# Optimization experiments

Hardware: AMD Instinct MI355X
Metric: run time of the kernel (lower is better)

## Reference

```python
import jax, jax.numpy as jnp
import numpy as np

N = 100000   # nodes
E = 640000   # directed edges
D = 128      # feature dim
C = 2        # classes


def setup_inputs() -> dict:
    key = jax.random.key(0)
    ks = jax.random.split(key, 7)
    s = 1.0 / np.sqrt(D)
    return {
        "x": jax.random.normal(ks[0], (N, D), jnp.float32),
        "edge_index": jax.random.randint(ks[1], (2, E), 0, N, jnp.int32),
        "W1": jax.random.normal(ks[2], (D, D), jnp.float32) * s,
        "b1": jnp.zeros((D,), jnp.float32),
        "W2": jax.random.normal(ks[3], (D, D), jnp.float32) * s,
        "b2": jnp.zeros((D,), jnp.float32),
        "Wfc": jax.random.normal(ks[4], (D, C), jnp.float32) * s,
        "bfc": jnp.zeros((C,), jnp.float32),
    }


def _gcn_conv(h, src, dst, W, b, n):
    """PyG GCNConv: y = D^{-1/2}(A+I)D^{-1/2} (h @ W) + b."""
    h = h @ W  # [N, D_out]
    loop = jnp.arange(n, dtype=src.dtype)
    s = jnp.concatenate([src, loop])
    d = jnp.concatenate([dst, loop])
    # degree of (A + I) counted at destination
    deg = jax.ops.segment_sum(jnp.ones_like(d, jnp.float32), d, num_segments=n)
    dinv = jax.lax.rsqrt(jnp.maximum(deg, 1.0))  # deg >= 1 via self loops
    norm = dinv[s] * dinv[d]                      # [E+N]
    msg = h[s] * norm[:, None]                    # gather + scale
    out = jax.ops.segment_sum(msg, d, num_segments=n)  # scatter-add
    return out + b


def reference(x, edge_index, W1, b1, W2, b2, Wfc, bfc):
    src, dst = edge_index[0], edge_index[1]
    n = x.shape[0]
    h = jax.nn.relu(_gcn_conv(x, src, dst, W1, b1, n))  # dropout = identity (eval)
    h = jax.nn.relu(_gcn_conv(h, src, dst, W2, b2, n))
    return h @ Wfc + bfc  # [N, 2] logits
```

## Files before the change

### kernel.cpp

```cpp
#include <hip/hip_runtime.h>
#include <hip/hip_bf16.h>

#define D 128
#define NBUCKET 64
#define BCAP 16384

typedef __bf16 bf16x8 __attribute__((ext_vector_type(8)));
typedef float f32x4 __attribute__((ext_vector_type(4)));


__global__ void prep_kernel(const float* __restrict__ W1, const float* __restrict__ W2,
                            __bf16* __restrict__ pw, int* __restrict__ bucket_cursor,
                            int* __restrict__ deghist, int* __restrict__ degcur) {
    int b = blockIdx.x;
    if (b < 128) {
        int t = b * 256 + threadIdx.x;
        int which = t >> 14, idx = t & 16383;
        const float* W = which ? W2 : W1;
        float w = W[idx];
        int k = idx >> 7, nn = idx & 127;
        int ks = which ? (((k & 15) << 3) | (k >> 4)) : k;
        int ntile = nn >> 4, nl = nn & 15;
        int kchunk = ks >> 5, quad = (ks >> 3) & 3, j = ks & 7;
        int o = (((ntile * 4 + kchunk) * 64 + quad * 16 + nl) << 3) + j;
        pw[(size_t)which * 16384 + o] = (__bf16)w;
    } else {
        int t = threadIdx.x;
        if (t < NBUCKET) bucket_cursor[t] = 0;
        else if (t < 128) deghist[t - 64] = 0;
        else if (t < 192) degcur[t - 128] = 0;
    }
}

__global__ void mega1_kernel(const float* __restrict__ X, const __bf16* __restrict__ PW,
                             __bf16* __restrict__ Zs, int nrows, int gb,
                             const int* __restrict__ src, const int* __restrict__ dst,
                             int* __restrict__ bucket_cursor, int2* __restrict__ bucket_edges,
                             int e, int bucketW) {
    __shared__ __align__(16) char smem[32768];
    int t = threadIdx.x;
    int b = blockIdx.x;
    if (b >= gb) {
        int* hist = (int*)smem;
        int* gbase = hist + 64;
        if (t < NBUCKET) hist[t] = 0;
        __syncthreads();
        int i0 = ((b - gb) * 256 + t) * 4;
        int sv[4], dv[4], bk[4], ls[4];
        int nv = 0;
        if (i0 + 4 <= e) {
            int4 s4 = *(const int4*)(src + i0);
            int4 d4 = *(const int4*)(dst + i0);
            sv[0] = s4.x; sv[1] = s4.y; sv[2] = s4.z; sv[3] = s4.w;
            dv[0] = d4.x; dv[1] = d4.y; dv[2] = d4.z; dv[3] = d4.w;
            nv = 4;
        } else {
            for (int i = i0; i < e; i++) { sv[nv] = src[i]; dv[nv] = dst[i]; nv++; }
        }
        for (int u = 0; u < nv; u++) {
            bk[u] = dv[u] / bucketW;
            ls[u] = atomicAdd(&hist[bk[u]], 1);
        }
        __syncthreads();
        if (t < NBUCKET) gbase[t] = atomicAdd(&bucket_cursor[t], hist[t]);
        __syncthreads();
        for (int u = 0; u < nv; u++) {
            int pos = bk[u] * BCAP + gbase[bk[u]] + ls[u];
            bucket_edges[pos] = make_int2(sv[u], dv[u]);
        }
        return;
    }
    bf16x8* sB = (bf16x8*)smem;
    const bf16x8* PW8 = (const bf16x8*)PW;
#pragma unroll
    for (int i = 0; i < 8; i++) sB[t + 256 * i] = PW8[t + 256 * i];

    int wave = t >> 6, lane = t & 63;
    int qm = lane & 15, quad = lane >> 4;
    int r0 = b * 64 + wave * 16;
    int row = r0 + qm;
    bool valid = row < nrows;
    const float* xr = X + (size_t)row * D + quad * 8;

    bf16x8 ahi[4], alo[4];
#pragma unroll
    for (int c = 0; c < 4; c++) {
        float4 zf = {0.f, 0.f, 0.f, 0.f};
        float4 xa = valid ? ((const float4*)(xr + c * 32))[0] : zf;
        float4 xb = valid ? ((const float4*)(xr + c * 32))[1] : zf;
        float xs[8] = {xa.x, xa.y, xa.z, xa.w, xb.x, xb.y, xb.z, xb.w};
        bf16x8 h, l;
#pragma unroll
        for (int j = 0; j < 8; j++) {
            float v = xs[j];
            __bf16 hh = (__bf16)v;
            h[j] = hh;
            l[j] = (__bf16)(v - (float)hh);
        }
        ahi[c] = h; alo[c] = l;
    }

    f32x4 acc[8];
#pragma unroll
    for (int nt = 0; nt < 8; nt++) acc[nt] = (f32x4){0.f, 0.f, 0.f, 0.f};

    __syncthreads();

#pragma unroll
    for (int c = 0; c < 4; c++) {
#pragma unroll
        for (int nt = 0; nt < 8; nt++) {
            bf16x8 bb = sB[(nt * 4 + c) * 64 + lane];
            acc[nt] = __builtin_amdgcn_mfma_f32_16x16x32_bf16(ahi[c], bb, acc[nt], 0, 0, 0);
            acc[nt] = __builtin_amdgcn_mfma_f32_16x16x32_bf16(alo[c], bb, acc[nt], 0, 0, 0);
        }
    }

#pragma unroll
    for (int reg = 0; reg < 4; reg++) {
        int orow = r0 + quad * 4 + reg;
        if (orow < nrows) {
            bf16x8 o;
#pragma unroll
            for (int nt = 0; nt < 8; nt++) o[nt] = (__bf16)acc[nt][reg];
            *(bf16x8*)(Zs + (size_t)orow * D + qm * 8) = o;
        }
    }
}

__global__ void count2_kernel(const int2* __restrict__ bucket_edges,
                              const int* __restrict__ bucket_cursor,
                              int* __restrict__ counts, float* __restrict__ dinv,
                              int* __restrict__ partial, int* __restrict__ deghist,
                              int n, int bucketW, int subW) {
    __shared__ int bins[400];
    __shared__ int sm[256];
    __shared__ int hb[64];
    int b = blockIdx.x, t = threadIdx.x;
    int bk = b >> 2, j = b & 3;
    int ns = bk * bucketW + j * subW;
    int be = min((bk + 1) * bucketW, n);
    int ne = min(ns + subW, be);
    int w = ne - ns;
    if (w <= 0) { if (t == 0) partial[b] = 0; return; }
    for (int i = t; i < w; i += 256) bins[i] = 0;
    if (t < 64) hb[t] = 0;
    __syncthreads();
    int m = bucket_cursor[bk];
    const int2* eb = bucket_edges + (size_t)bk * BCAP;
    for (int i = t; i < m; i += 256) {
        int d = eb[i].y;
        if (d >= ns && d < ne) atomicAdd(&bins[d - ns], 1);
    }
    __syncthreads();
    int s = 0;
    for (int i = t; i < w; i += 256) {
        int c = bins[i];
        counts[ns + i] = c;
        dinv[ns + i] = rsqrtf((float)(c + 1));
        atomicAdd(&hb[min(c, 63)], 1);
        s += c;
    }
    sm[t] = s; __syncthreads();
    for (int off = 128; off > 0; off >>= 1) { if (t < off) sm[t] += sm[t + off]; __syncthreads(); }
    if (t == 0) partial[b] = sm[0];
    if (t < 64 && hb[t]) atomicAdd(&deghist[t], hb[t]);
}

__global__ void scanfill_kernel(const int2* __restrict__ bucket_edges,
                                const int* __restrict__ bucket_cursor,
                                const int* __restrict__ counts,
                                const int* __restrict__ partial,
                                const int* __restrict__ deghist,
                                int* __restrict__ row_ptr, int* __restrict__ csr,
                                int* __restrict__ degcur, int* __restrict__ order,
                                int n, int bucketW, int subW) {
    __shared__ int cur[400];
    __shared__ int sm[256];
    __shared__ int hb2[64];
    __shared__ int gb2[64];
    __shared__ int dgex[64];
    __shared__ int pexs;
    int b = blockIdx.x, t = threadIdx.x;
    int bk = b >> 2, j = b & 3;
    int ns = bk * bucketW + j * subW;
    int be = min((bk + 1) * bucketW, n);
    int ne = min(ns + subW, be);
    int w = ne - ns;
    if (w <= 0) return;
    int pv = partial[t];
    sm[t] = pv; __syncthreads();
    for (int off = 1; off < 256; off <<= 1) {
        int u = (t >= off) ? sm[t - off] : 0;
        __syncthreads();
        sm[t] += u;
        __syncthreads();
    }
    if (t == b) pexs = sm[t] - pv;
    __syncthreads();
    int pbase = pexs;
    int dh = (t < 64) ? deghist[t] : 0;
    sm[t] = dh; __syncthreads();
    for (int off = 1; off < 64; off <<= 1) {
        int u = (t >= off && t < 64) ? sm[t - off] : 0;
        __syncthreads();
        if (t < 64) sm[t] += u;
        __syncthreads();
    }
    if (t < 64) { dgex[t] = sm[t] - dh; hb2[t] = 0; }
    __syncthreads();
    int i0 = t * 2;
    int c0 = (i0 < w) ? counts[ns + i0] : 0;
    int c1 = (i0 + 1 < w) ? counts[ns + i0 + 1] : 0;
    sm[t] = c0 + c1; __syncthreads();
    int own = c0 + c1;
    for (int off = 1; off < 256; off <<= 1) {
        int u = (t >= off) ? sm[t - off] : 0;
        __syncthreads();
        sm[t] += u;
        __syncthreads();
    }
    int base = pbase + sm[t] - own;
    if (i0 < w)     { row_ptr[ns + i0] = base;          cur[i0] = base; }
    if (i0 + 1 < w) { row_ptr[ns + i0 + 1] = base + c0; cur[i0 + 1] = base + c0; }
    int bin0 = min(c0, 63), bin1 = min(c1, 63);
    int r0 = (i0 < w) ? atomicAdd(&hb2[bin0], 1) : 0;
    int r1 = (i0 + 1 < w) ? atomicAdd(&hb2[bin1], 1) : 0;
    __syncthreads();
    if (t < 64 && hb2[t]) gb2[t] = atomicAdd(&degcur[t], hb2[t]);
    __syncthreads();
    if (i0 < w)     order[dgex[bin0] + gb2[bin0] + r0] = ns + i0;
    if (i0 + 1 < w) order[dgex[bin1] + gb2[bin1] + r1] = ns + i0 + 1;
    __syncthreads();
    int m = bucket_cursor[bk];
    const int2* eb = bucket_edges + (size_t)bk * BCAP;
    for (int i = t; i < m; i += 256) {
        int2 ed = eb[i];
        if (ed.y >= ns && ed.y < ne) {
            int pos = atomicAdd(&cur[ed.y - ns], 1);
            csr[pos] = ed.x;
        }
    }
}

__global__ void agg1_gemm2_kernel(const __bf16* __restrict__ Zs, const int* __restrict__ row_ptr,
                                  const int* __restrict__ counts, const int* __restrict__ csr,
                                  const float* __restrict__ dinv, const float* __restrict__ bias,
                                  const __bf16* __restrict__ PW, const int* __restrict__ order,
                                  __bf16* __restrict__ Z2, int n) {
    __shared__ __align__(16) __bf16 sH[32 * 128];
    __shared__ bf16x8 sBp[512];
    int t = threadIdx.x;
    const bf16x8* PW8 = (const bf16x8*)PW;

    int gbase = blockIdx.x * 32;
    int grp = t >> 4, c = t & 15;

    float bs[8];
#pragma unroll
    for (int j = 0; j < 8; j++) bs[j] = bias[j * 16 + c];

    const bf16x8* Z8 = (const bf16x8*)Zs;
    for (int r = 0; r < 4; r++) {
        int lr = r * 8 + grp;
        int idx = gbase + lr;
        bf16x8 o = {};
        if (idx < n) {
            int v = order[(n - 1) - idx];
            float dv = dinv[v];
            bf16x8 zc = Z8[(size_t)v * 16 + c];
            float sw = dv * dv;
            float acc[8];
#pragma unroll
            for (int j = 0; j < 8; j++) acc[j] = (float)zc[j] * sw;
            int start = row_ptr[v], cnt = counts[v];
            int i = 0;
            if (cnt >= 4) {
                int s0 = csr[start], s1 = csr[start + 1];
                int s2 = csr[start + 2], s3 = csr[start + 3];
                for (; i + 8 <= cnt; i += 4) {
                    int t0 = csr[start + i + 4], t1 = csr[start + i + 5];
                    int t2 = csr[start + i + 6], t3 = csr[start + i + 7];
                    bf16x8 m0 = Z8[(size_t)s0 * 16 + c];
                    bf16x8 m1 = Z8[(size_t)s1 * 16 + c];
                    bf16x8 m2 = Z8[(size_t)s2 * 16 + c];
                    bf16x8 m3 = Z8[(size_t)s3 * 16 + c];
                    float w0 = dinv[s0] * dv, w1 = dinv[s1] * dv;
                    float w2 = dinv[s2] * dv, w3 = dinv[s3] * dv;
#pragma unroll
                    for (int j = 0; j < 8; j++) acc[j] = fmaf(w0, (float)m0[j], acc[j]);
#pragma unroll
                    for (int j = 0; j < 8; j++) acc[j] = fmaf(w1, (float)m1[j], acc[j]);
#pragma unroll
                    for (int j = 0; j < 8; j++) acc[j] = fmaf(w2, (float)m2[j], acc[j]);
#pragma unroll
                    for (int j = 0; j < 8; j++) acc[j] = fmaf(w3, (float)m3[j], acc[j]);
                    s0 = t0; s1 = t1; s2 = t2; s3 = t3;
                }
                {
                    bf16x8 m0 = Z8[(size_t)s0 * 16 + c];
                    bf16x8 m1 = Z8[(size_t)s1 * 16 + c];
                    bf16x8 m2 = Z8[(size_t)s2 * 16 + c];
                    bf16x8 m3 = Z8[(size_t)s3 * 16 + c];
                    float w0 = dinv[s0] * dv, w1 = dinv[s1] * dv;
                    float w2 = dinv[s2] * dv, w3 = dinv[s3] * dv;
#pragma unroll
                    for (int j = 0; j < 8; j++) acc[j] = fmaf(w0, (float)m0[j], acc[j]);
#pragma unroll
                    for (int j = 0; j < 8; j++) acc[j] = fmaf(w1, (float)m1[j], acc[j]);
#pragma unroll
                    for (int j = 0; j < 8; j++) acc[j] = fmaf(w2, (float)m2[j], acc[j]);
#pragma unroll
                    for (int j = 0; j < 8; j++) acc[j] = fmaf(w3, (float)m3[j], acc[j]);
                    i += 4;
                }
            }
            for (; i < cnt; i++) {
                int s0 = csr[start + i];
                float w0 = dinv[s0] * dv;
                bf16x8 m0 = Z8[(size_t)s0 * 16 + c];
#pragma unroll
                for (int j = 0; j < 8; j++) acc[j] = fmaf(w0, (float)m0[j], acc[j]);
            }
#pragma unroll
            for (int j = 0; j < 8; j++) o[j] = (__bf16)fmaxf(acc[j] + bs[j], 0.f);
        }
        *(bf16x8*)(sH + lr * 128 + ((c ^ (lr & 7)) << 3)) = o;
    }

    int wave = t >> 6, lane = t & 63;
    int qm = lane & 15, quad = lane >> 4;
    int lrow = wave * 16 + qm;

    f32x4 acc[8];
#pragma unroll
    for (int nt = 0; nt < 8; nt++) acc[nt] = (f32x4){0.f, 0.f, 0.f, 0.f};

#pragma unroll
    for (int cc = 0; cc < 4; cc++) {
        __syncthreads();
#pragma unroll
        for (int i = 0; i < 4; i++) {
            int idx = i * 128 + t;
            sBp[idx] = PW8[((idx >> 6) * 4 + cc) * 64 + (idx & 63)];
        }
        int slot = quad + cc * 4;
        bf16x8 a = *(const bf16x8*)(sH + lrow * 128 + ((slot ^ (lrow & 7)) << 3));
        __syncthreads();
#pragma unroll
        for (int nt = 0; nt < 8; nt++) {
            bf16x8 bb = sBp[nt * 64 + lane];
            acc[nt] = __builtin_amdgcn_mfma_f32_16x16x32_bf16(a, bb, acc[nt], 0, 0, 0);
        }
    }

#pragma unroll
    for (int reg = 0; reg < 4; reg++) {
        int lrr = wave * 16 + quad * 4 + reg;
        int gidx = gbase + lrr;
        if (gidx < n) {
            int v = order[(n - 1) - gidx];
            float sc = dinv[v];
            bf16x8 o;
#pragma unroll
            for (int nt = 0; nt < 8; nt++) o[nt] = (__bf16)(acc[nt][reg] * sc);
            *(bf16x8*)(Z2 + (size_t)v * D + qm * 8) = o;
        }
    }
}

__global__ void agg2_fc_kernel(const __bf16* __restrict__ Zs, const int* __restrict__ row_ptr,
                               const int* __restrict__ counts, const int* __restrict__ csr,
                               const float* __restrict__ dinv, const float* __restrict__ bias,
                               const float* __restrict__ Wfc, const float* __restrict__ bfc,
                               const int* __restrict__ order, float* __restrict__ out, int n) {
    int t = blockIdx.x * 256 + threadIdx.x;
    int idx = t >> 4, c = t & 15;
    if (idx >= n) return;
    int v = order[(n - 1) - idx];
    float dv = dinv[v];
    const bf16x8* Z8 = (const bf16x8*)Zs;
    bf16x8 zc = Z8[(size_t)v * 16 + c];
    float acc[8];
#pragma unroll
    for (int j = 0; j < 8; j++) acc[j] = (float)zc[j];
    int start = row_ptr[v], cnt = counts[v];
    int i = 0;
    if (cnt >= 4) {
        int s0 = csr[start], s1 = csr[start + 1];
        int s2 = csr[start + 2], s3 = csr[start + 3];
        for (; i + 8 <= cnt; i += 4) {
            int t0 = csr[start + i + 4], t1 = csr[start + i + 5];
            int t2 = csr[start + i + 6], t3 = csr[start + i + 7];
            bf16x8 m0 = Z8[(size_t)s0 * 16 + c];
            bf16x8 m1 = Z8[(size_t)s1 * 16 + c];
            bf16x8 m2 = Z8[(size_t)s2 * 16 + c];
            bf16x8 m3 = Z8[(size_t)s3 * 16 + c];
#pragma unroll
            for (int j = 0; j < 8; j++) acc[j] += (float)m0[j];
#pragma unroll
            for (int j = 0; j < 8; j++) acc[j] += (float)m1[j];
#pragma unroll
            for (int j = 0; j < 8; j++) acc[j] += (float)m2[j];
#pragma unroll
            for (int j = 0; j < 8; j++) acc[j] += (float)m3[j];
            s0 = t0; s1 = t1; s2 = t2; s3 = t3;
        }
        {
            bf16x8 m0 = Z8[(size_t)s0 * 16 + c];
            bf16x8 m1 = Z8[(size_t)s1 * 16 + c];
            bf16x8 m2 = Z8[(size_t)s2 * 16 + c];
            bf16x8 m3 = Z8[(size_t)s3 * 16 + c];
#pragma unroll
            for (int j = 0; j < 8; j++) acc[j] += (float)m0[j];
#pragma unroll
            for (int j = 0; j < 8; j++) acc[j] += (float)m1[j];
#pragma unroll
            for (int j = 0; j < 8; j++) acc[j] += (float)m2[j];
#pragma unroll
            for (int j = 0; j < 8; j++) acc[j] += (float)m3[j];
            i += 4;
        }
    }
    for (; i < cnt; i++) {
        int s0 = csr[start + i];
        bf16x8 m0 = Z8[(size_t)s0 * 16 + c];
#pragma unroll
        for (int j = 0; j < 8; j++) acc[j] += (float)m0[j];
    }
    float a0 = 0.f, a1 = 0.f;
#pragma unroll
    for (int j = 0; j < 8; j++) {
        int p = j * 16 + c;
        float hj = fmaxf(fmaf(dv, acc[j], bias[p]), 0.f);
        a0 = fmaf(hj, Wfc[p * 2], a0);
        a1 = fmaf(hj, Wfc[p * 2 + 1], a1);
    }
#pragma unroll
    for (int off = 8; off > 0; off >>= 1) {
        a0 += __shfl_down(a0, off, 16);
        a1 += __shfl_down(a1, off, 16);
    }
    if (c == 0) {
        out[(size_t)v * 2 + 0] = a0 + bfc[0];
        out[(size_t)v * 2 + 1] = a1 + bfc[1];
    }
}


extern "C" void kernel_launch(void* const* d_in, const int* in_sizes, int n_in,
                              void* d_out, int out_size, void* d_ws, size_t ws_size,
                              hipStream_t stream) {
    const float* x   = (const float*)d_in[0];
    const int*   ei  = (const int*)d_in[1];
    const float* W1  = (const float*)d_in[2];
    const float* b1  = (const float*)d_in[3];
    const float* W2  = (const float*)d_in[4];
    const float* b2  = (const float*)d_in[5];
    const float* Wfc = (const float*)d_in[6];
    const float* bfc = (const float*)d_in[7];
    float* out = (float*)d_out;

    int n = in_sizes[0] / D;
    int e = in_sizes[1] / 2;
    const int* src = ei;
    const int* dst = ei + e;

    int bucketW = (n + NBUCKET - 1) / NBUCKET;
    int subW = (bucketW + 3) / 4;

    char* ws = (char*)d_ws;
    size_t nb = (size_t)n * 4;
    int*    counts  = (int*)(ws);
    float*  dinv    = (float*)(ws + nb);
    int*    rowptr  = (int*)(ws + 2 * nb);
    int*    partial = (int*)(ws + 3 * nb);
    int*    bcur    = (int*)(ws + 3 * nb + 1024);
    int*    deghist = (int*)(ws + 3 * nb + 1280);
    int*    degcur  = (int*)(ws + 3 * nb + 1536);
    int*    order   = (int*)(ws + 3 * nb + 2048);
    int2*   bedges  = (int2*)(ws + 4 * nb + 2048);
    size_t  off1    = 4 * nb + 2048 + (size_t)NBUCKET * BCAP * 8;
    int*    csr     = (int*)(ws + off1);
    __bf16* pw      = (__bf16*)(ws + off1 + (size_t)e * 4);
    __bf16* z1      = (__bf16*)(ws + off1 + (size_t)e * 4 + 65536);
    __bf16* z2      = z1 + (size_t)n * D;

    int eab = ((e + 3) / 4 + 255) / 256;
    int gb  = (n + 63) / 64;
    int gb2 = (n + 31) / 32;
    int ab  = ((n * 16) + 255) / 256;

    prep_kernel<<<129, 256, 0, stream>>>(W1, W2, pw, bcur, deghist, degcur);
    mega1_kernel<<<gb + eab, 256, 0, stream>>>(x, pw, z1, n, gb, src, dst,
                                               bcur, bedges, e, bucketW);
    count2_kernel<<<256, 256, 0, stream>>>(bedges, bcur, counts, dinv, partial, deghist,
                                           n, bucketW, subW);
    scanfill_kernel<<<256, 256, 0, stream>>>(bedges, bcur, counts, partial, deghist,
                                             rowptr, csr, degcur, order, n, bucketW, subW);
    agg1_gemm2_kernel<<<gb2, 128, 0, stream>>>(z1, rowptr, counts, csr, dinv, b1,
                                               pw + 16384, order, z2, n);
    agg2_fc_kernel<<<ab, 256, 0, stream>>>(z2, rowptr, counts, csr, dinv, b2, Wfc, bfc,
                                           order, out, n);
}
```

Measured before the change: 232.6 us.

## Split GEMM1 across count and scanfill kernels to overlap with CSR build

The first-layer GEMM moves out of the edge-bucketing kernel. Its row blocks are split in half and appended to the degree-count kernel and the scan/fill kernel, so the compute-heavy GEMM runs alongside the small, latency-bound CSR construction stages. Weight packing is merged into the edge-bucketing kernel, and the counter zeroing that prep_kernel used to do is now a hipMemsetAsync. The intent is to fill idle compute units during the 256-block graph stages. In exchange, the 32KB shared allocation now applies to the count and scan blocks too, and the memset adds a separate operation to the stream.

After: 234.4 us. No clear change (+0.8%).

```diff
diff --git a/kernel.cpp b/kernel.cpp
--- a/kernel.cpp
+++ b/kernel.cpp
@@ -9,13 +9,16 @@
 typedef float f32x4 __attribute__((ext_vector_type(4)));
 
 
-__global__ void prep_kernel(const float* __restrict__ W1, const float* __restrict__ W2,
-                            __bf16* __restrict__ pw, int* __restrict__ bucket_cursor,
-                            int* __restrict__ deghist, int* __restrict__ degcur) {
+__global__ void combo_kernel(const float* __restrict__ W1, const float* __restrict__ W2,
+                             __bf16* __restrict__ pw,
+                             const int* __restrict__ src, const int* __restrict__ dst,
+                             int* __restrict__ bucket_cursor, int2* __restrict__ bucket_edges,
+                             int e, int bucketW) {
     int b = blockIdx.x;
+    int t = threadIdx.x;
     if (b < 128) {
-        int t = b * 256 + threadIdx.x;
-        int which = t >> 14, idx = t & 16383;
+        int tt = b * 256 + t;
+        int which = tt >> 14, idx = tt & 16383;
         const float* W = which ? W2 : W1;
         float w = W[idx];
         int k = idx >> 7, nn = idx & 127;
@@ -24,52 +27,41 @@
         int kchunk = ks >> 5, quad = (ks >> 3) & 3, j = ks & 7;
         int o = (((ntile * 4 + kchunk) * 64 + quad * 16 + nl) << 3) + j;
         pw[(size_t)which * 16384 + o] = (__bf16)w;
+        return;
+    }
+    __shared__ int hist[NBUCKET];
+    __shared__ int gbase[NBUCKET];
+    if (t < NBUCKET) hist[t] = 0;
+    __syncthreads();
+    int i0 = ((b - 128) * 256 + t) * 4;
+    int sv[4], dv[4], bk[4], ls[4];
+    int nv = 0;
+    if (i0 + 4 <= e) {
+        int4 s4 = *(const int4*)(src + i0);
+        int4 d4 = *(const int4*)(dst + i0);
+        sv[0] = s4.x; sv[1] = s4.y; sv[2] = s4.z; sv[3] = s4.w;
+        dv[0] = d4.x; dv[1] = d4.y; dv[2] = d4.z; dv[3] = d4.w;
+        nv = 4;
     } else {
-        int t = threadIdx.x;
-        if (t < NBUCKET) bucket_cursor[t] = 0;
-        else if (t < 128) deghist[t - 64] = 0;
-        else if (t < 192) degcur[t - 128] = 0;
-    }
-}
-
-__global__ void mega1_kernel(const float* __restrict__ X, const __bf16* __restrict__ PW,
-                             __bf16* __restrict__ Zs, int nrows, int gb,
-                             const int* __restrict__ src, const int* __restrict__ dst,
-                             int* __restrict__ bucket_cursor, int2* __restrict__ bucket_edges,
-                             int e, int bucketW) {
-    __shared__ __align__(16) char smem[32768];
-    int t = threadIdx.x;
-    int b = blockIdx.x;
-    if (b >= gb) {
-        int* hist = (int*)smem;
-        int* gbase = hist + 64;
-        if (t < NBUCKET) hist[t] = 0;
-        __syncthreads();
-        int i0 = ((b - gb) * 256 + t) * 4;
-        int sv[4], dv[4], bk[4], ls[4];
-        int nv = 0;
-        if (i0 + 4 <= e) {
-            int4 s4 = *(const int4*)(src + i0);
-            int4 d4 = *(const int4*)(dst + i0);
-            sv[0] = s4.x; sv[1] = s4.y; sv[2] = s4.z; sv[3] = s4.w;
-            dv[0] = d4.x; dv[1] = d4.y; dv[2] = d4.z; dv[3] = d4.w;
-            nv = 4;
-        } else {
-            for (int i = i0; i < e; i++) { sv[nv] = src[i]; dv[nv] = dst[i]; nv++; }
-        }
-        for (int u = 0; u < nv; u++) {
-            bk[u] = dv[u] / bucketW;
-            ls[u] = atomicAdd(&hist[bk[u]], 1);
-        }
-        __syncthreads();
-        if (t < NBUCKET) gbase[t] = atomicAdd(&bucket_cursor[t], hist[t]);
-        __syncthreads();
-        for (int u = 0; u < nv; u++) {
-            int pos = bk[u] * BCAP + gbase[bk[u]] + ls[u];
-            bucket_edges[pos] = make_int2(sv[u], dv[u]);
-        }
-        return;
-    }
+        for (int i = i0; i < e; i++) { sv[nv] = src[i]; dv[nv] = dst[i]; nv++; }
+    }
+    for (int u = 0; u < nv; u++) {
+        bk[u] = dv[u] / bucketW;
+        ls[u] = atomicAdd(&hist[bk[u]], 1);
+    }
+    __syncthreads();
+    if (t < NBUCKET) gbase[t] = atomicAdd(&bucket_cursor[t], hist[t]);
+    __syncthreads();
+    for (int u = 0; u < nv; u++) {
+        int pos = bk[u] * BCAP + gbase[bk[u]] + ls[u];
+        bucket_edges[pos] = make_int2(sv[u], dv[u]);
+    }
+}
+
+__device__ __forceinline__ void gemm1_body(char* smem, int t, int gbk,
+                                           const float* __restrict__ X,
+                                           const __bf16* __restrict__ PW,
+                                           __bf16* __restrict__ Zs, int n) {
     bf16x8* sB = (bf16x8*)smem;
     const bf16x8* PW8 = (const bf16x8*)PW;
 #pragma unroll
@@ -77,9 +69,9 @@
 
     int wave = t >> 6, lane = t & 63;
     int qm = lane & 15, quad = lane >> 4;
-    int r0 = b * 64 + wave * 16;
+    int r0 = gbk * 64 + wave * 16;
     int row = r0 + qm;
-    bool valid = row < nrows;
+    bool valid = row < n;
     const float* xr = X + (size_t)row * D + quad * 8;
 
     bf16x8 ahi[4], alo[4];
@@ -119,7 +111,7 @@
 #pragma unroll
     for (int reg = 0; reg < 4; reg++) {
         int orow = r0 + quad * 4 + reg;
-        if (orow < nrows) {
+        if (orow < n) {
             bf16x8 o;
 #pragma unroll
             for (int nt = 0; nt < 8; nt++) o[nt] = (__bf16)acc[nt][reg];
@@ -128,119 +120,133 @@
     }
 }
 
-__global__ void count2_kernel(const int2* __restrict__ bucket_edges,
+__global__ void mega_a_kernel(const int2* __restrict__ bucket_edges,
                               const int* __restrict__ bucket_cursor,
                               int* __restrict__ counts, float* __restrict__ dinv,
                               int* __restrict__ partial, int* __restrict__ deghist,
+                              const float* __restrict__ X, const __bf16* __restrict__ PW,
+                              __bf16* __restrict__ Zs,
                               int n, int bucketW, int subW) {
-    __shared__ int bins[400];
-    __shared__ int sm[256];
-    __shared__ int hb[64];
+    __shared__ __align__(16) char smem[32768];
     int b = blockIdx.x, t = threadIdx.x;
-    int bk = b >> 2, j = b & 3;
-    int ns = bk * bucketW + j * subW;
-    int be = min((bk + 1) * bucketW, n);
-    int ne = min(ns + subW, be);
-    int w = ne - ns;
-    if (w <= 0) { if (t == 0) partial[b] = 0; return; }
-    for (int i = t; i < w; i += 256) bins[i] = 0;
-    if (t < 64) hb[t] = 0;
-    __syncthreads();
-    int m = bucket_cursor[bk];
-    const int2* eb = bucket_edges + (size_t)bk * BCAP;
-    for (int i = t; i < m; i += 256) {
-        int d = eb[i].y;
-        if (d >= ns && d < ne) atomicAdd(&bins[d - ns], 1);
-    }
-    __syncthreads();
-    int s = 0;
-    for (int i = t; i < w; i += 256) {
-        int c = bins[i];
-        counts[ns + i] = c;
-        dinv[ns + i] = rsqrtf((float)(c + 1));
-        atomicAdd(&hb[min(c, 63)], 1);
-        s += c;
-    }
-    sm[t] = s; __syncthreads();
-    for (int off = 128; off > 0; off >>= 1) { if (t < off) sm[t] += sm[t + off]; __syncthreads(); }
-    if (t == 0) partial[b] = sm[0];
-    if (t < 64 && hb[t]) atomicAdd(&deghist[t], hb[t]);
-}
-
-__global__ void scanfill_kernel(const int2* __restrict__ bucket_edges,
-                                const int* __restrict__ bucket_cursor,
-                                const int* __restrict__ counts,
-                                const int* __restrict__ partial,
-                                const int* __restrict__ deghist,
-                                int* __restrict__ row_ptr, int* __restrict__ csr,
-                                int* __restrict__ degcur, int* __restrict__ order,
-                                int n, int bucketW, int subW) {
-    __shared__ int cur[400];
-    __shared__ int sm[256];
-    __shared__ int hb2[64];
-    __shared__ int gb2[64];
-    __shared__ int dgex[64];
-    __shared__ int pexs;
+    if (b < 256) {
+        int* bins = (int*)smem;
+        int* sm   = bins + 400;
+        int* hb   = sm + 256;
+        int bk = b >> 2, j = b & 3;
+        int ns = bk * bucketW + j * subW;
+        int be = min((bk + 1) * bucketW, n);
+        int ne = min(ns + subW, be);
+        int w = ne - ns;
+        if (w <= 0) { if (t == 0) partial[b] = 0; return; }
+        for (int i = t; i < w; i += 256) bins[i] = 0;
+        if (t < 64) hb[t] = 0;
+        __syncthreads();
+        int m = bucket_cursor[bk];
+        const int2* eb = bucket_edges + (size_t)bk * BCAP;
+        for (int i = t; i < m; i += 256) {
+            int d = eb[i].y;
+            if (d >= ns && d < ne) atomicAdd(&bins[d - ns], 1);
+        }
+        __syncthreads();
+        int s = 0;
+        for (int i = t; i < w; i += 256) {
+            int c = bins[i];
+            counts[ns + i] = c;
+            dinv[ns + i] = rsqrtf((float)(c + 1));
+            atomicAdd(&hb[min(c, 63)], 1);
+            s += c;
+        }
+        sm[t] = s; __syncthreads();
+        for (int off = 128; off > 0; off >>= 1) { if (t < off) sm[t] += sm[t + off]; __syncthreads(); }
+        if (t == 0) partial[b] = sm[0];
+        if (t < 64 && hb[t]) atomicAdd(&deghist[t], hb[t]);
+        return;
+    }
+    gemm1_body(smem, t, b - 256, X, PW, Zs, n);
+}
+
+__global__ void mega_b_kernel(const int2* __restrict__ bucket_edges,
+                              const int* __restrict__ bucket_cursor,
+                              const int* __restrict__ counts,
+                              const int* __restrict__ partial,
+                              const int* __restrict__ deghist,
+                              int* __restrict__ row_ptr, int* __restrict__ csr,
+                              int* __restrict__ degcur, int* __restrict__ order,
+                              const float* __restrict__ X, const __bf16* __restrict__ PW,
+                              __bf16* __restrict__ Zs,
+                              int n, int bucketW, int subW, int gba) {
+    __shared__ __align__(16) char smem[32768];
     int b = blockIdx.x, t = threadIdx.x;
-    int bk = b >> 2, j = b & 3;
-    int ns = bk * bucketW + j * subW;
-    int be = min((bk + 1) * bucketW, n);
-    int ne = min(ns + subW, be);
-    int w = ne - ns;
-    if (w <= 0) return;
-    int pv = partial[t];
-    sm[t] = pv; __syncthreads();
-    for (int off = 1; off < 256; off <<= 1) {
-        int u = (t >= off) ? sm[t - off] : 0;
-        __syncthreads();
-        sm[t] += u;
-        __syncthreads();
-    }
-    if (t == b) pexs = sm[t] - pv;
-    __syncthreads();
-    int pbase = pexs;
-    int dh = (t < 64) ? deghist[t] : 0;
-    sm[t] = dh; __syncthreads();
-    for (int off = 1; off < 64; off <<= 1) {
-        int u = (t >= off && t < 64) ? sm[t - off] : 0;
-        __syncthreads();
-        if (t < 64) sm[t] += u;
-        __syncthreads();
-    }
-    if (t < 64) { dgex[t] = sm[t] - dh; hb2[t] = 0; }
-    __syncthreads();
-    int i0 = t * 2;
-    int c0 = (i0 < w) ? counts[ns + i0] : 0;
-    int c1 = (i0 + 1 < w) ? counts[ns + i0 + 1] : 0;
-    sm[t] = c0 + c1; __syncthreads();
-    int own = c0 + c1;
-    for (int off = 1; off < 256; off <<= 1) {
-        int u = (t >= off) ? sm[t - off] : 0;
-        __syncthreads();
-        sm[t] += u;
-        __syncthreads();
-    }
-    int base = pbase + sm[t] - own;
-    if (i0 < w)     { row_ptr[ns + i0] = base;          cur[i0] = base; }
-    if (i0 + 1 < w) { row_ptr[ns + i0 + 1] = base + c0; cur[i0 + 1] = base + c0; }
-    int bin0 = min(c0, 63), bin1 = min(c1, 63);
-    int r0 = (i0 < w) ? atomicAdd(&hb2[bin0], 1) : 0;
-    int r1 = (i0 + 1 < w) ? atomicAdd(&hb2[bin1], 1) : 0;
-    __syncthreads();
-    if (t < 64 && hb2[t]) gb2[t] = atomicAdd(&degcur[t], hb2[t]);
-    __syncthreads();
-    if (i0 < w)     order[dgex[bin0] + gb2[bin0] + r0] = ns + i0;
-    if (i0 + 1 < w) order[dgex[bin1] + gb2[bin1] + r1] = ns + i0 + 1;
-    __syncthreads();
-    int m = bucket_cursor[bk];
-    const int2* eb = bucket_edges + (size_t)bk * BCAP;
-    for (int i = t; i < m; i += 256) {
-        int2 ed = eb[i];
-        if (ed.y >= ns && ed.y < ne) {
-            int pos = atomicAdd(&cur[ed.y - ns], 1);
-            csr[pos] = ed.x;
-        }
-    }
+    if (b < 256) {
+        int* cur  = (int*)smem;
+        int* sm   = cur + 400;
+        int* hb2  = sm + 256;
+        int* gb2  = hb2 + 64;
+        int* dgex = gb2 + 64;
+        int* pexs = dgex + 64;
+        int bk = b >> 2, j = b & 3;
+        int ns = bk * bucketW + j * subW;
+        int be = min((bk + 1) * bucketW, n);
+        int ne = min(ns + subW, be);
+        int w = ne - ns;
+        if (w <= 0) return;
+        int pv = partial[t];
+        sm[t] = pv; __syncthreads();
+        for (int off = 1; off < 256; off <<= 1) {
+            int u = (t >= off) ? sm[t - off] : 0;
+            __syncthreads();
+            sm[t] += u;
+            __syncthreads();
+        }
+        if (t == b) pexs[0] = sm[t] - pv;
+        __syncthreads();
+        int pbase = pexs[0];
+        int dh = (t < 64) ? deghist[t] : 0;
+        sm[t] = dh; __syncthreads();
+        for (int off = 1; off < 64; off <<= 1) {
+            int u = (t >= off && t < 64) ? sm[t - off] : 0;
+            __syncthreads();
+            if (t < 64) sm[t] += u;
+            __syncthreads();
+        }
+        if (t < 64) { dgex[t] = sm[t] - dh; hb2[t] = 0; }
+        __syncthreads();
+        int i0 = t * 2;
+        int c0 = (i0 < w) ? counts[ns + i0] : 0;
+        int c1 = (i0 + 1 < w) ? counts[ns + i0 + 1] : 0;
+        sm[t] = c0 + c1; __syncthreads();
+        int own = c0 + c1;
+        for (int off = 1; off < 256; off <<= 1) {
+            int u = (t >= off) ? sm[t - off] : 0;
+            __syncthreads();
+            sm[t] += u;
+            __syncthreads();
+        }
+        int base = pbase + sm[t] - own;
+        if (i0 < w)     { row_ptr[ns + i0] = base;          cur[i0] = base; }
+        if (i0 + 1 < w) { row_ptr[ns + i0 + 1] = base + c0; cur[i0 + 1] = base + c0; }
+        int bin0 = min(c0, 63), bin1 = min(c1, 63);
+        int r0 = (i0 < w) ? atomicAdd(&hb2[bin0], 1) : 0;
+        int r1 = (i0 + 1 < w) ? atomicAdd(&hb2[bin1], 1) : 0;
+        __syncthreads();
+        if (t < 64 && hb2[t]) gb2[t] = atomicAdd(&degcur[t], hb2[t]);
+        __syncthreads();
+        if (i0 < w)     order[dgex[bin0] + gb2[bin0] + r0] = ns + i0;
+        if (i0 + 1 < w) order[dgex[bin1] + gb2[bin1] + r1] = ns + i0 + 1;
+        __syncthreads();
+        int m = bucket_cursor[bk];
+        const int2* eb = bucket_edges + (size_t)bk * BCAP;
+        for (int i = t; i < m; i += 256) {
+            int2 ed = eb[i];
+            if (ed.y >= ns && ed.y < ne) {
+                int pos = atomicAdd(&cur[ed.y - ns], 1);
+                csr[pos] = ed.x;
+            }
+        }
+        return;
+    }
+    gemm1_body(smem, t, gba + (b - 256), X, PW, Zs, n);
 }
 
 __global__ void agg1_gemm2_kernel(const __bf16* __restrict__ Zs, const int* __restrict__ row_ptr,
@@ -488,16 +494,19 @@
 
     int eab = ((e + 3) / 4 + 255) / 256;
     int gb  = (n + 63) / 64;
+    int gba = (gb + 1) / 2;
+    int gbb = gb - gba;
     int gb2 = (n + 31) / 32;
     int ab  = ((n * 16) + 255) / 256;
 
-    prep_kernel<<<129, 256, 0, stream>>>(W1, W2, pw, bcur, deghist, degcur);
-    mega1_kernel<<<gb + eab, 256, 0, stream>>>(x, pw, z1, n, gb, src, dst,
-                                               bcur, bedges, e, bucketW);
-    count2_kernel<<<256, 256, 0, stream>>>(bedges, bcur, counts, dinv, partial, deghist,
-                                           n, bucketW, subW);
-    scanfill_kernel<<<256, 256, 0, stream>>>(bedges, bcur, counts, partial, deghist,
-                                             rowptr, csr, degcur, order, n, bucketW, subW);
+    hipMemsetAsync(ws + 3 * nb + 1024, 0, 768, stream);
+    combo_kernel<<<128 + eab, 256, 0, stream>>>(W1, W2, pw, src, dst, bcur, bedges,
+                                                e, bucketW);
+    mega_a_kernel<<<256 + gba, 256, 0, stream>>>(bedges, bcur, counts, dinv, partial,
+                                                 deghist, x, pw, z1, n, bucketW, subW);
+    mega_b_kernel<<<256 + gbb, 256, 0, stream>>>(bedges, bcur, counts, partial, deghist,
+                                                 rowptr, csr, degcur, order, x, pw, z1,
+                                                 n, bucketW, subW, gba);
     agg1_gemm2_kernel<<<gb2, 128, 0, stream>>>(z1, rowptr, counts, csr, dinv, b1,
                                                pw + 16384, order, z2, n);
     agg2_fc_kernel<<<ab, 256, 0, stream>>>(z2, rowptr, counts, csr, dinv, b2, Wfc, bfc,
```
